# Optimization experiments

Measured on AMD Instinct MI355X. Metric: run time of the kernel, lower is better.

Reference implementation:

```python
import jax, jax.numpy as jnp
import numpy as np

V, E, HD, C, B, T = 30000, 256, 512, 9, 128, 256
H = HD // 2  # per-direction hidden size


def setup_inputs() -> dict:
    key = jax.random.key(0)
    ks = iter(jax.random.split(key, 64))

    def rn(shape, scale):
        return jax.random.normal(next(ks), shape, jnp.float32) * scale

    s = 1.0 / np.sqrt(H)
    inp = {}
    inp["x"] = jax.random.randint(next(ks), (B, T), 0, V, dtype=jnp.int32)
    inp["tags"] = jax.random.randint(next(ks), (B, T), 0, C, dtype=jnp.int32)
    inp["mask"] = jnp.ones((B, T), dtype=bool)
    inp["emb"] = rn((V, E), 1.0)
    in_dims = [E, HD]
    for l in range(2):
        for d in ("f", "b"):
            inp[f"w_ih_l{l}{d}"] = rn((4 * H, in_dims[l]), s)
            inp[f"w_hh_l{l}{d}"] = rn((4 * H, H), s)
            inp[f"b_ih_l{l}{d}"] = rn((4 * H,), s)
            inp[f"b_hh_l{l}{d}"] = rn((4 * H,), s)
    inp["lin_w"] = rn((C, HD), 1.0 / np.sqrt(HD))
    inp["lin_b"] = rn((C,), 0.01)
    inp["trans"] = rn((C, C), 0.1)
    inp["start"] = rn((C,), 0.1)
    inp["end"] = rn((C,), 0.1)
    return inp


def _lstm_dir(x, w_ih, w_hh, b_ih, b_hh):
    # x: [T, B, in]; PyTorch gate order i, f, g, o
    Bn = x.shape[1]
    Hn = w_hh.shape[1]

    def step(carry, xt):
        h, c = carry
        g = xt @ w_ih.T + b_ih + h @ w_hh.T + b_hh
        i, f, gg, o = jnp.split(g, 4, axis=-1)
        c = jax.nn.sigmoid(f) * c + jax.nn.sigmoid(i) * jnp.tanh(gg)
        h = jax.nn.sigmoid(o) * jnp.tanh(c)
        return (h, c), h

    z = jnp.zeros((Bn, Hn), x.dtype)
    _, hs = jax.lax.scan(step, (z, z), x)
    return hs  # [T, B, H]


def _bilstm(x, pf, pb):
    hf = _lstm_dir(x, *pf)
    hb = _lstm_dir(x[::-1], *pb)[::-1]
    return jnp.concatenate([hf, hb], axis=-1)  # [T, B, 2H]


def _crf_nll(em, tags, mask, trans, start, end):
    # em: [T, B, C] (time-major emissions); tags, mask: [B, T]
    tags_t = tags.T              # [T, B]
    mf = mask.astype(em.dtype).T  # [T, B]
    Bn = tags.shape[0]
    bidx = jnp.arange(Bn)
    # numerator: score of the gold path
    num = start[tags_t[0]] + em[0, bidx, tags_t[0]]
    step_em = jnp.take_along_axis(em[1:], tags_t[1:, :, None], axis=2)[..., 0]  # [T-1, B]
    step_sc = trans[tags_t[:-1], tags_t[1:]] + step_em
    num = num + (step_sc * mf[1:]).sum(0)
    lengths = mask.sum(1).astype(jnp.int32)
    last_tags = tags[bidx, lengths - 1]
    num = num + end[last_tags]
    # denominator: forward algorithm (logsumexp scan over time)
    alpha0 = start + em[0]  # [B, C]

    def step(alpha, inp):
        e, m = inp
        nxt = jax.nn.logsumexp(alpha[:, :, None] + trans[None] + e[:, None, :], axis=1)
        return jnp.where(m[:, None] > 0, nxt, alpha), None

    alpha, _ = jax.lax.scan(step, alpha0, (em[1:], mf[1:]))
    logZ = jax.nn.logsumexp(alpha + end, axis=1)
    return -(num - logZ).mean()


def reference(x, tags, mask, emb,
              w_ih_l0f, w_hh_l0f, b_ih_l0f, b_hh_l0f,
              w_ih_l0b, w_hh_l0b, b_ih_l0b, b_hh_l0b,
              w_ih_l1f, w_hh_l1f, b_ih_l1f, b_hh_l1f,
              w_ih_l1b, w_hh_l1b, b_ih_l1b, b_hh_l1b,
              lin_w, lin_b, trans, start, end):
    xt = emb[x].transpose(1, 0, 2)  # [T, B, E]
    h1 = _bilstm(xt, (w_ih_l0f, w_hh_l0f, b_ih_l0f, b_hh_l0f),
                 (w_ih_l0b, w_hh_l0b, b_ih_l0b, b_hh_l0b))
    h2 = _bilstm(h1, (w_ih_l1f, w_hh_l1f, b_ih_l1f, b_hh_l1f),
                 (w_ih_l1b, w_hh_l1b, b_ih_l1b, b_hh_l1b))
    em = h2 @ lin_w.T + lin_b  # [T, B, C]
    return _crf_nll(em, tags, mask, trans, start, end)
```

## Files before the change

kernel.cpp:

```cpp
#include <hip/hip_runtime.h>

#define T_LEN 256
#define B_SZ  128
#define E_DIM 256
#define NC    9

typedef short bf16x8 __attribute__((ext_vector_type(8)));
typedef float f32x4  __attribute__((ext_vector_type(4)));
typedef unsigned short u16x4 __attribute__((ext_vector_type(4)));
typedef unsigned int   u32x2 __attribute__((ext_vector_type(2)));

__device__ __forceinline__ float bf2f(unsigned short u) {
    return __uint_as_float(((unsigned)u) << 16);
}
__device__ __forceinline__ unsigned short f2bf(float f) {
    unsigned x = __float_as_uint(f);
    unsigned r = x + 0x7FFFu + ((x >> 16) & 1u);
    return (unsigned short)(r >> 16);
}
__device__ __forceinline__ float rcpf(float x) { return __builtin_amdgcn_rcpf(x); }
__device__ __forceinline__ float sigf(float x) { return rcpf(1.0f + __expf(-x)); }
__device__ __forceinline__ float tanh_fast(float x) {
    float e = __expf(2.0f * x);
    return 1.0f - 2.0f * rcpf(e + 1.0f);
}

__global__ void k_prep(const float* __restrict__ i0f, const float* __restrict__ i0b,
                       const float* __restrict__ i1f, const float* __restrict__ i1b,
                       const float* __restrict__ h0, const float* __restrict__ h1,
                       const float* __restrict__ h2, const float* __restrict__ h3,
                       unsigned short* __restrict__ d0f, unsigned short* __restrict__ d0b,
                       unsigned short* __restrict__ d1f, unsigned short* __restrict__ d1b,
                       unsigned short* __restrict__ p0, unsigned short* __restrict__ p1,
                       unsigned short* __restrict__ p2, unsigned short* __restrict__ p3) {
    int j = blockIdx.y;
    int idx = blockIdx.x * 256 + threadIdx.x;
    if (j < 4) {
        int n = (j < 2) ? 262144 : 524288;
        if (idx < n) {
            const float* s = (j == 0) ? i0f : (j == 1) ? i0b : (j == 2) ? i1f : i1b;
            unsigned short* d = (j == 0) ? d0f : (j == 1) ? d0b : (j == 2) ? d1f : d1b;
            d[idx] = f2bf(s[idx]);
        }
    } else {
        if (idx < 262144) {
            const float* s = (j == 4) ? h0 : (j == 5) ? h1 : (j == 6) ? h2 : h3;
            unsigned short* d = (j == 4) ? p0 : (j == 5) ? p1 : (j == 6) ? p2 : p3;
            int p = idx >> 8, k = idx & 255;
            int srow = ((p >> 4) & 3) * 256 + (p >> 9) * 128 + ((p >> 6) & 7) * 16 + (p & 15);
            d[idx] = f2bf(s[srow * 256 + k]);
        }
    }
}

__global__ void k_bias4(const float* __restrict__ a0, const float* __restrict__ b0,
                        const float* __restrict__ a1, const float* __restrict__ b1,
                        const float* __restrict__ a2, const float* __restrict__ b2,
                        const float* __restrict__ a3, const float* __restrict__ b3,
                        float* __restrict__ d) {
    int idx = blockIdx.x * 256 + threadIdx.x;
    if (idx < 4096) {
        int j = idx >> 10, i = idx & 1023;
        const float* a = (j == 0) ? a0 : (j == 1) ? a1 : (j == 2) ? a2 : a3;
        const float* b = (j == 0) ? b0 : (j == 1) ? b1 : (j == 2) ? b2 : b3;
        d[idx] = a[i] + b[i];
    }
}

__global__ void k_init(unsigned* __restrict__ c) {
    int i = blockIdx.x * 256 + threadIdx.x;
    if (i < 2048)
        __hip_atomic_store(c + i, 0u, __ATOMIC_RELAXED, __HIP_MEMORY_SCOPE_AGENT);
}

__global__ void k_embed(const int* __restrict__ x, const float* __restrict__ emb,
                        unsigned short* __restrict__ X0) {
    int row = blockIdx.x * 4 + (threadIdx.x >> 6);
    int lane = threadIdx.x & 63;
    int t = row >> 7, b = row & 127;
    int xi = x[b * T_LEN + t];
    const float4 e = *reinterpret_cast<const float4*>(emb + (size_t)xi * E_DIM + lane * 4);
    ushort4 o;
    o.x = f2bf(e.x); o.y = f2bf(e.y); o.z = f2bf(e.z); o.w = f2bf(e.w);
    *reinterpret_cast<ushort4*>(X0 + (size_t)row * E_DIM + lane * 4) = o;
}

template<int K>
__global__ __launch_bounds__(256, 1) void k_gemm2(const unsigned short* __restrict__ A,
                                                  const unsigned short* __restrict__ W,
                                                  const float* __restrict__ bias,
                                                  unsigned short* __restrict__ out) {
    int m0 = blockIdx.x * 128;
    int w = threadIdx.x >> 6, l = threadIdx.x & 63;
    int lr = l & 15, hi = l >> 4;
    bf16x8 af[2][K / 32];
#pragma unroll
    for (int s = 0; s < 2; s++)
#pragma unroll
        for (int kk = 0; kk < K / 32; kk++)
            af[s][kk] = *reinterpret_cast<const bf16x8*>(
                A + (size_t)(m0 + w * 32 + s * 16 + lr) * K + kk * 32 + hi * 8);
#pragma unroll 1
    for (int tn = 0; tn < 16; tn++) {
        int n0 = tn * 64;
        f32x4 acc[4][2];
        f32x4 z = {0.f, 0.f, 0.f, 0.f};
#pragma unroll
        for (int c = 0; c < 4; c++) { acc[c][0] = z; acc[c][1] = z; }
#pragma unroll
        for (int kk = 0; kk < K / 32; kk++) {
#pragma unroll
            for (int c = 0; c < 4; c++) {
                bf16x8 wf = *reinterpret_cast<const bf16x8*>(
                    W + (size_t)(n0 + c * 16 + lr) * K + kk * 32 + hi * 8);
                acc[c][0] = __builtin_amdgcn_mfma_f32_16x16x32_bf16(wf, af[0][kk], acc[c][0], 0, 0, 0);
                acc[c][1] = __builtin_amdgcn_mfma_f32_16x16x32_bf16(wf, af[1][kk], acc[c][1], 0, 0, 0);
            }
        }
#pragma unroll
        for (int c = 0; c < 4; c++) {
            float4 bv = *reinterpret_cast<const float4*>(bias + n0 + c * 16 + hi * 4);
#pragma unroll
            for (int s = 0; s < 2; s++) {
                unsigned short hb[4];
                hb[0] = f2bf(acc[c][s][0] + bv.x);
                hb[1] = f2bf(acc[c][s][1] + bv.y);
                hb[2] = f2bf(acc[c][s][2] + bv.z);
                hb[3] = f2bf(acc[c][s][3] + bv.w);
                u32x2 dv;
                dv[0] = (unsigned)hb[0] | ((unsigned)hb[1] << 16);
                dv[1] = (unsigned)hb[2] | ((unsigned)hb[3] << 16);
                *reinterpret_cast<u32x2*>(out + (size_t)(m0 + w * 32 + s * 16 + lr) * 1024
                                          + n0 + c * 16 + hi * 4) = dv;
            }
        }
    }
}

__global__ __launch_bounds__(512, 1) void k_lstm7(const unsigned short* __restrict__ Gf,
                                                  const unsigned short* __restrict__ Gb,
                                                  const unsigned short* __restrict__ Wpf,
                                                  const unsigned short* __restrict__ Wpb,
                                                  unsigned short* __restrict__ Hout,
                                                  unsigned* __restrict__ flags_base) {
    __shared__ unsigned short smem[12288];
    unsigned short* gin_lds = smem;
    unsigned short* h_lds = smem + 8192;

    int bx = blockIdx.x;
    int dir = (bx >> 3) & 1, rg = bx & 7, sidx = bx >> 4;
    const unsigned short* G = dir ? Gb : Gf;
    const unsigned short* Wp = dir ? Wpb : Wpf;

    unsigned long long myflag = (unsigned long long)(uintptr_t)(flags_base + bx * 16);
    unsigned long long pflag  = (unsigned long long)(uintptr_t)(flags_base + (bx ^ 16) * 16);

    int tid = threadIdx.x;
    int w = tid >> 6, l = tid & 63;
    int lr = l & 15, hi = l >> 4;
    int hc4 = sidx * 128 + w * 16 + hi * 4;

    bf16x8 wfr[4][8];
    {
        const unsigned short* wbase = Wp + (size_t)(sidx * 8 + w) * 64 * 256;
#pragma unroll
        for (int g = 0; g < 4; g++)
#pragma unroll
            for (int kk = 0; kk < 8; kk++)
                wfr[g][kk] = *reinterpret_cast<const bf16x8*>(
                    wbase + (size_t)(g * 16 + lr) * 256 + kk * 32 + hi * 8);
    }

    int Xr = (lr & 7) << 4;
    int goff[2];
#pragma unroll
    for (int p = 0; p < 2; p++) {
        int off = (p * 512 + tid) * 16;
        int row = off >> 10, inrow = off & 1023;
        int g = inrow >> 8, cb = inrow & 255;
        int Xs = (row & 7) << 4;
        goff[p] = (rg * 16 + row) * 1024 + ((g * 512 + sidx * 256 + (cb ^ Xs)) >> 1);
    }
    int phoff = 0;
    {
        int off = (tid & 255) * 16;
        int prow = off >> 8, pin = off & 255;
        int Xs = (prow & 7) << 4;
        phoff = (rg * 16 + prow) * 512 + dir * 256 + (sidx ^ 1) * 128 + ((pin ^ Xs) >> 1);
    }
    int lofs[8];
#pragma unroll
    for (int kk = 0; kk < 8; kk++) {
        int cb = kk * 64 + hi * 16;
        lofs[kk] = (cb >> 8) * 4096 + lr * 256 + ((cb & 255) ^ Xr);
    }
    int wofs = sidx * 4096 + lr * 256 + ((w * 32 + hi * 8) ^ Xr);
    int gofs[4];
#pragma unroll
    for (int g = 0; g < 4; g++) gofs[g] = lr * 1024 + g * 256 + ((w * 32 + hi * 8) ^ Xr);

    int t0 = dir ? (T_LEN - 1) : 0;
    long dg = dir ? -(long)(B_SZ * 1024) : (long)(B_SZ * 1024);
    long dh = dir ? -(long)(B_SZ * 512)  : (long)(B_SZ * 512);
    const unsigned short* Gt  = G + (size_t)t0 * (B_SZ * 1024);
    const unsigned short* Hpt = Hout + (size_t)t0 * (B_SZ * 512);
    unsigned short* hst = Hout + ((size_t)t0 * B_SZ + rg * 16 + lr) * 512 + dir * 256 + hc4;

    float c4[4] = {0.f, 0.f, 0.f, 0.f};
    f32x4 z = {0.f, 0.f, 0.f, 0.f};

    for (int s = 0; s < T_LEN; s++) {
        __builtin_amdgcn_global_load_lds(
            (const __attribute__((address_space(1))) unsigned int*)(Gt + goff[0]),
            (__attribute__((address_space(3))) unsigned int*)(gin_lds + w * 512), 16, 0, 0);
        __builtin_amdgcn_global_load_lds(
            (const __attribute__((address_space(1))) unsigned int*)(Gt + goff[1]),
            (__attribute__((address_space(3))) unsigned int*)(gin_lds + 4096 + w * 512), 16, 0, 0);

        if (s == 0) {
            *reinterpret_cast<int4*>((char*)h_lds + tid * 16) = make_int4(0, 0, 0, 0);
        } else {
            if (tid == 0) {
                unsigned v;
                for (;;) {
                    asm volatile("global_load_dword %0, %1, off sc1\n\ts_waitcnt vmcnt(0)"
                                 : "=v"(v) : "v"(pflag) : "memory");
                    if (v >= (unsigned)s) break;
                    __builtin_amdgcn_s_sleep(1);
                }
            }
            __syncthreads();
            if (tid < 256) {
                __builtin_amdgcn_global_load_lds(
                    (const __attribute__((address_space(1))) unsigned int*)(Hpt + phoff),
                    (__attribute__((address_space(3))) unsigned int*)(h_lds + (sidx ^ 1) * 2048 + w * 512),
                    16, 0, 0);
            }
            Hpt += dh;
        }
        asm volatile("s_waitcnt vmcnt(0)" ::: "memory");
        __syncthreads();

        bf16x8 hf[8];
#pragma unroll
        for (int kk = 0; kk < 8; kk++)
            hf[kk] = *reinterpret_cast<const bf16x8*>((char*)h_lds + lofs[kk]);
        f32x4 acc[4];
#pragma unroll
        for (int g = 0; g < 4; g++) acc[g] = z;
#pragma unroll
        for (int g = 0; g < 4; g++)
#pragma unroll
            for (int kk = 0; kk < 8; kk++)
                acc[g] = __builtin_amdgcn_mfma_f32_16x16x32_bf16(wfr[g][kk], hf[kk], acc[g], 0, 0, 0);
        __syncthreads();

        u16x4 g4[4];
#pragma unroll
        for (int g = 0; g < 4; g++)
            g4[g] = *reinterpret_cast<const u16x4*>((char*)gin_lds + gofs[g]);
        unsigned short hb[4];
#pragma unroll
        for (int r = 0; r < 4; r++) {
            float xi = acc[0][r] + bf2f(g4[0][r]);
            float xf = acc[1][r] + bf2f(g4[1][r]);
            float xg = acc[2][r] + bf2f(g4[2][r]);
            float xo = acc[3][r] + bf2f(g4[3][r]);
            float cv = sigf(xf) * c4[r] + sigf(xi) * tanh_fast(xg);
            c4[r] = cv;
            hb[r] = f2bf(sigf(xo) * tanh_fast(cv));
        }
        u32x2 dv;
        dv[0] = (unsigned)hb[0] | ((unsigned)hb[1] << 16);
        dv[1] = (unsigned)hb[2] | ((unsigned)hb[3] << 16);
        *reinterpret_cast<u32x2*>((char*)h_lds + wofs) = dv;
        unsigned long long saddr = (unsigned long long)(uintptr_t)hst;
        asm volatile("global_store_dwordx2 %0, %1, off sc1" :: "v"(saddr), "v"(dv));
        hst += dh;

        asm volatile("s_waitcnt vmcnt(0)" ::: "memory");
        __syncthreads();
        if (tid == 0) {
            unsigned val = (unsigned)(s + 1);
            asm volatile("global_store_dword %0, %1, off sc1" :: "v"(myflag), "v"(val));
        }
        Gt += dg;
    }
}

__global__ __launch_bounds__(256) void k_emis(const unsigned short* __restrict__ H2,
                                              const float* __restrict__ lw,
                                              const float* __restrict__ lb,
                                              float* __restrict__ EM) {
    int row = blockIdx.x * 4 + (threadIdx.x >> 6);
    int lane = threadIdx.x & 63;
    bf16x8 hv = *reinterpret_cast<const bf16x8*>(H2 + (size_t)row * 512 + lane * 8);
    float hf[8];
#pragma unroll
    for (int j = 0; j < 8; j++) hf[j] = bf2f((unsigned short)hv[j]);
#pragma unroll
    for (int cc = 0; cc < NC; cc++) {
        const float* wr = lw + cc * 512 + lane * 8;
        float4 w0 = *reinterpret_cast<const float4*>(wr);
        float4 w1 = *reinterpret_cast<const float4*>(wr + 4);
        float d = hf[0] * w0.x + hf[1] * w0.y + hf[2] * w0.z + hf[3] * w0.w +
                  hf[4] * w1.x + hf[5] * w1.y + hf[6] * w1.z + hf[7] * w1.w;
#pragma unroll
        for (int off = 32; off >= 1; off >>= 1) d += __shfl_down(d, off, 64);
        if (lane == 0) EM[(size_t)row * NC + cc] = d + lb[cc];
    }
}

__global__ __launch_bounds__(64) void k_crf(const float* __restrict__ EM,
                                            const int* __restrict__ tags,
                                            const float* __restrict__ trans,
                                            const float* __restrict__ start,
                                            const float* __restrict__ end,
                                            float* __restrict__ partials) {
    int b = blockIdx.x, tid = threadIdx.x;
    __shared__ float tr[160];
    for (int i = tid; i < 160; i += 64) tr[i] = (i < 81) ? trans[i] : 0.f;
    __syncthreads();

    int j = tid;
    float alpha = -1e30f;
    if (j < 9) alpha = start[j] + EM[b * NC + j];

    for (int t = 1; t < T_LEN; t++) {
        float av[9];
#pragma unroll
        for (int i = 0; i < 9; i++) av[i] = __shfl(alpha, i, 64) + tr[i * 9 + j];
        float m = av[0];
#pragma unroll
        for (int i = 1; i < 9; i++) m = fmaxf(m, av[i]);
        float sum = 0.f;
#pragma unroll
        for (int i = 0; i < 9; i++) sum += expf(av[i] - m);
        float e = (j < 9) ? EM[(size_t)t * (B_SZ * NC) + b * NC + j] : 0.f;
        float na = m + logf(sum) + e;
        alpha = (j < 9) ? na : -1e30f;
    }
    float aend[9];
    float m2 = -1e30f;
#pragma unroll
    for (int i = 0; i < 9; i++) {
        aend[i] = __shfl(alpha, i, 64) + end[i];
        m2 = fmaxf(m2, aend[i]);
    }
    float s2 = 0.f;
#pragma unroll
    for (int i = 0; i < 9; i++) s2 += expf(aend[i] - m2);
    float logZ = m2 + logf(s2);

    float nsum = 0.f;
    for (int t = 1 + tid; t < T_LEN; t += 64) {
        int tp = tags[b * T_LEN + t - 1], tc = tags[b * T_LEN + t];
        nsum += tr[tp * 9 + tc] + EM[(size_t)t * (B_SZ * NC) + b * NC + tc];
    }
#pragma unroll
    for (int off = 32; off >= 1; off >>= 1) nsum += __shfl_down(nsum, off, 64);

    if (tid == 0) {
        int t0 = tags[b * T_LEN], tl = tags[b * T_LEN + T_LEN - 1];
        float num = start[t0] + EM[b * NC + t0] + nsum + end[tl];
        partials[b] = num - logZ;
    }
}

__global__ void k_reduce(const float* __restrict__ partials, float* __restrict__ out) {
    int tid = threadIdx.x;
    float v = partials[tid];
#pragma unroll
    for (int off = 32; off >= 1; off >>= 1) v += __shfl_down(v, off, 64);
    __shared__ float sm[2];
    if ((tid & 63) == 0) sm[tid >> 6] = v;
    __syncthreads();
    if (tid == 0) out[0] = -(sm[0] + sm[1]) / 128.0f;
}

extern "C" void kernel_launch(void* const* d_in, const int* in_sizes, int n_in,
                              void* d_out, int out_size, void* d_ws, size_t ws_size,
                              hipStream_t stream) {
    const int*   x     = (const int*)d_in[0];
    const int*   tags  = (const int*)d_in[1];
    const float* emb   = (const float*)d_in[3];
    const float* w_ih[4] = {(const float*)d_in[4],  (const float*)d_in[8],
                            (const float*)d_in[12], (const float*)d_in[16]};
    const float* w_hh[4] = {(const float*)d_in[5],  (const float*)d_in[9],
                            (const float*)d_in[13], (const float*)d_in[17]};
    const float* b_ih[4] = {(const float*)d_in[6],  (const float*)d_in[10],
                            (const float*)d_in[14], (const float*)d_in[18]};
    const float* b_hh[4] = {(const float*)d_in[7],  (const float*)d_in[11],
                            (const float*)d_in[15], (const float*)d_in[19]};
    const float* lin_w = (const float*)d_in[20];
    const float* lin_b = (const float*)d_in[21];
    const float* trans = (const float*)d_in[22];
    const float* start = (const float*)d_in[23];
    const float* endv  = (const float*)d_in[24];

    char* ws = (char*)d_ws;
    size_t off = 0;
    auto alloc = [&](size_t bytes) -> void* {
        size_t a = (off + 255) & ~(size_t)255;
        off = a + bytes;
        return (void*)(ws + a);
    };

    unsigned short* wb_ih0f = (unsigned short*)alloc(1024 * 256 * 2);
    unsigned short* wb_ih0b = (unsigned short*)alloc(1024 * 256 * 2);
    unsigned short* wb_ih1f = (unsigned short*)alloc(1024 * 512 * 2);
    unsigned short* wb_ih1b = (unsigned short*)alloc(1024 * 512 * 2);
    unsigned short* wp0f = (unsigned short*)alloc(1024 * 256 * 2);
    unsigned short* wp0b = (unsigned short*)alloc(1024 * 256 * 2);
    unsigned short* wp1f = (unsigned short*)alloc(1024 * 256 * 2);
    unsigned short* wp1b = (unsigned short*)alloc(1024 * 256 * 2);
    float* bsum = (float*)alloc(4096 * 4);
    unsigned short* X0 = (unsigned short*)alloc((size_t)32768 * 256 * 2);
    unsigned short* Gf = (unsigned short*)alloc((size_t)32768 * 1024 * 2);
    unsigned short* Gb = (unsigned short*)alloc((size_t)32768 * 1024 * 2);
    unsigned short* H1 = (unsigned short*)alloc((size_t)32768 * 512 * 2);
    unsigned short* H2 = (unsigned short*)alloc((size_t)32768 * 512 * 2);
    float* EM = (float*)alloc((size_t)32768 * NC * 4);
    float* partials = (float*)alloc(128 * 4);
    unsigned* ctrs = (unsigned*)alloc(8192);

    hipLaunchKernelGGL(k_init, dim3(8), dim3(256), 0, stream, ctrs);

    hipLaunchKernelGGL(k_prep, dim3(2048, 8), dim3(256), 0, stream,
                       w_ih[0], w_ih[1], w_ih[2], w_ih[3],
                       w_hh[0], w_hh[1], w_hh[2], w_hh[3],
                       wb_ih0f, wb_ih0b, wb_ih1f, wb_ih1b,
                       wp0f, wp0b, wp1f, wp1b);
    hipLaunchKernelGGL(k_bias4, dim3(16), dim3(256), 0, stream,
                       b_ih[0], b_hh[0], b_ih[1], b_hh[1],
                       b_ih[2], b_hh[2], b_ih[3], b_hh[3], bsum);

    hipLaunchKernelGGL(k_embed, dim3(8192), dim3(256), 0, stream, x, emb, X0);

    hipLaunchKernelGGL(k_gemm2<256>, dim3(256), dim3(256), 0, stream, X0, wb_ih0f, bsum, Gf);
    hipLaunchKernelGGL(k_gemm2<256>, dim3(256), dim3(256), 0, stream, X0, wb_ih0b, bsum + 1024, Gb);
    hipLaunchKernelGGL(k_lstm7, dim3(32), dim3(512), 0, stream, Gf, Gb, wp0f, wp0b, H1, ctrs);

    hipLaunchKernelGGL(k_gemm2<512>, dim3(256), dim3(256), 0, stream, H1, wb_ih1f, bsum + 2048, Gf);
    hipLaunchKernelGGL(k_gemm2<512>, dim3(256), dim3(256), 0, stream, H1, wb_ih1b, bsum + 3072, Gb);
    hipLaunchKernelGGL(k_lstm7, dim3(32), dim3(512), 0, stream, Gf, Gb, wp1f, wp1b, H2, ctrs + 1024);

    hipLaunchKernelGGL(k_emis, dim3(8192), dim3(256), 0, stream, H2, lin_w, lin_b, EM);
    hipLaunchKernelGGL(k_crf, dim3(128), dim3(64), 0, stream, EM, tags, trans, start, endv, partials);
    hipLaunchKernelGGL(k_reduce, dim3(1), dim3(128), 0, stream, partials, (float*)d_out);
}
```

Before: 2.053 ms.

## Run each LSTM direction/row-group in one 1024-thread block, removing cross-block flags

The recurrent LSTM kernel previously split the hidden dimension across two 512-thread blocks that exchanged h through global memory with spin-wait flags every timestep. Now one 1024-thread block covers the full hidden size per (direction, row group), keeping h entirely in double-buffered LDS, and prefetches the next timestep's gate inputs into a second LDS buffer. This removes the per-step global flag polling, the h exchange, and the flag-init kernel, and it changes the recurrent weight permutation to match the new layout. In exchange only 16 blocks run, with higher register pressure per block and 80KB of LDS each.

```diff
diff --git a/kernel.cpp b/kernel.cpp
--- a/kernel.cpp
+++ b/kernel.cpp
@@ -47,7 +47,7 @@
             const float* s = (j == 4) ? h0 : (j == 5) ? h1 : (j == 6) ? h2 : h3;
             unsigned short* d = (j == 4) ? p0 : (j == 5) ? p1 : (j == 6) ? p2 : p3;
             int p = idx >> 8, k = idx & 255;
-            int srow = ((p >> 4) & 3) * 256 + (p >> 9) * 128 + ((p >> 6) & 7) * 16 + (p & 15);
+            int srow = ((p >> 4) & 3) * 256 + (p >> 6) * 16 + (p & 15);
             d[idx] = f2bf(s[srow * 256 + k]);
         }
     }
@@ -65,12 +65,6 @@
         const float* b = (j == 0) ? b0 : (j == 1) ? b1 : (j == 2) ? b2 : b3;
         d[idx] = a[i] + b[i];
     }
-}
-
-__global__ void k_init(unsigned* __restrict__ c) {
-    int i = blockIdx.x * 256 + threadIdx.x;
-    if (i < 2048)
-        __hip_atomic_store(c + i, 0u, __ATOMIC_RELAXED, __HIP_MEMORY_SCOPE_AGENT);
 }
 
 __global__ void k_embed(const int* __restrict__ x, const float* __restrict__ emb,
@@ -137,32 +131,27 @@
     }
 }
 
-__global__ __launch_bounds__(512, 1) void k_lstm7(const unsigned short* __restrict__ Gf,
-                                                  const unsigned short* __restrict__ Gb,
-                                                  const unsigned short* __restrict__ Wpf,
-                                                  const unsigned short* __restrict__ Wpb,
-                                                  unsigned short* __restrict__ Hout,
-                                                  unsigned* __restrict__ flags_base) {
-    __shared__ unsigned short smem[12288];
-    unsigned short* gin_lds = smem;
-    unsigned short* h_lds = smem + 8192;
+__global__ __launch_bounds__(1024, 1) void k_lstm8(const unsigned short* __restrict__ Gf,
+                                                   const unsigned short* __restrict__ Gb,
+                                                   const unsigned short* __restrict__ Wpf,
+                                                   const unsigned short* __restrict__ Wpb,
+                                                   unsigned short* __restrict__ Hout) {
+    __shared__ unsigned short smem[40960];
+    unsigned short* gbuf = smem;
+    unsigned short* hbuf = smem + 32768;
 
     int bx = blockIdx.x;
-    int dir = (bx >> 3) & 1, rg = bx & 7, sidx = bx >> 4;
+    int dir = bx >> 3, rg = bx & 7;
     const unsigned short* G = dir ? Gb : Gf;
     const unsigned short* Wp = dir ? Wpb : Wpf;
-
-    unsigned long long myflag = (unsigned long long)(uintptr_t)(flags_base + bx * 16);
-    unsigned long long pflag  = (unsigned long long)(uintptr_t)(flags_base + (bx ^ 16) * 16);
 
     int tid = threadIdx.x;
     int w = tid >> 6, l = tid & 63;
     int lr = l & 15, hi = l >> 4;
-    int hc4 = sidx * 128 + w * 16 + hi * 4;
 
     bf16x8 wfr[4][8];
     {
-        const unsigned short* wbase = Wp + (size_t)(sidx * 8 + w) * 64 * 256;
+        const unsigned short* wbase = Wp + (size_t)w * 64 * 256;
 #pragma unroll
         for (int g = 0; g < 4; g++)
 #pragma unroll
@@ -171,80 +160,60 @@
                     wbase + (size_t)(g * 16 + lr) * 256 + kk * 32 + hi * 8);
     }
 
-    int Xr = (lr & 7) << 4;
-    int goff[2];
-#pragma unroll
-    for (int p = 0; p < 2; p++) {
-        int off = (p * 512 + tid) * 16;
-        int row = off >> 10, inrow = off & 1023;
-        int g = inrow >> 8, cb = inrow & 255;
-        int Xs = (row & 7) << 4;
-        goff[p] = (rg * 16 + row) * 1024 + ((g * 512 + sidx * 256 + (cb ^ Xs)) >> 1);
-    }
-    int phoff = 0;
-    {
-        int off = (tid & 255) * 16;
-        int prow = off >> 8, pin = off & 255;
-        int Xs = (prow & 7) << 4;
-        phoff = (rg * 16 + prow) * 512 + dir * 256 + (sidx ^ 1) * 128 + ((pin ^ Xs) >> 1);
-    }
-    int lofs[8];
-#pragma unroll
-    for (int kk = 0; kk < 8; kk++) {
-        int cb = kk * 64 + hi * 16;
-        lofs[kk] = (cb >> 8) * 4096 + lr * 256 + ((cb & 255) ^ Xr);
-    }
-    int wofs = sidx * 4096 + lr * 256 + ((w * 32 + hi * 8) ^ Xr);
-    int gofs[4];
-#pragma unroll
-    for (int g = 0; g < 4; g++) gofs[g] = lr * 1024 + g * 256 + ((w * 32 + hi * 8) ^ Xr);
+    int off0 = tid * 16, off1 = 16384 + tid * 16;
+    int r0 = off0 >> 11, in0 = off0 & 2047;
+    int r1 = off1 >> 11, in1 = off1 & 2047;
+    int gsrc0 = (rg * 16 + r0) * 1024 + ((in0 ^ ((r0 & 7) << 4)) >> 1);
+    int gsrc1 = (rg * 16 + r1) * 1024 + ((in1 ^ ((r1 & 7) << 4)) >> 1);
+    int Xs = (lr & 7) << 4, Xh = (lr & 15) << 4;
+    int hfo[8];
+#pragma unroll
+    for (int kk = 0; kk < 8; kk++) hfo[kk] = lr * 512 + ((kk * 64 + hi * 16) ^ Xh);
+    int gro[4];
+#pragma unroll
+    for (int g = 0; g < 4; g++) gro[g] = lr * 2048 + ((g * 512 + w * 32 + hi * 8) ^ Xs);
+    int hwo = lr * 512 + ((w * 32 + hi * 8) ^ Xh);
 
     int t0 = dir ? (T_LEN - 1) : 0;
     long dg = dir ? -(long)(B_SZ * 1024) : (long)(B_SZ * 1024);
     long dh = dir ? -(long)(B_SZ * 512)  : (long)(B_SZ * 512);
-    const unsigned short* Gt  = G + (size_t)t0 * (B_SZ * 1024);
-    const unsigned short* Hpt = Hout + (size_t)t0 * (B_SZ * 512);
-    unsigned short* hst = Hout + ((size_t)t0 * B_SZ + rg * 16 + lr) * 512 + dir * 256 + hc4;
+    const unsigned short* G0 = G + (size_t)t0 * (B_SZ * 1024);
+    const unsigned short* Gpre = G0 + dg;
+    unsigned short* hst = Hout + ((size_t)t0 * B_SZ + rg * 16 + lr) * 512
+                          + dir * 256 + w * 16 + hi * 4;
+
+    *reinterpret_cast<int4*>((char*)hbuf + tid * 16) = make_int4(0, 0, 0, 0);
+    __builtin_amdgcn_global_load_lds(
+        (const __attribute__((address_space(1))) unsigned int*)(G0 + gsrc0),
+        (__attribute__((address_space(3))) unsigned int*)(gbuf + w * 512), 16, 0, 0);
+    __builtin_amdgcn_global_load_lds(
+        (const __attribute__((address_space(1))) unsigned int*)(G0 + gsrc1),
+        (__attribute__((address_space(3))) unsigned int*)(gbuf + 8192 + w * 512), 16, 0, 0);
+    __syncthreads();
 
     float c4[4] = {0.f, 0.f, 0.f, 0.f};
     f32x4 z = {0.f, 0.f, 0.f, 0.f};
 
-    for (int s = 0; s < T_LEN; s++) {
-        __builtin_amdgcn_global_load_lds(
-            (const __attribute__((address_space(1))) unsigned int*)(Gt + goff[0]),
-            (__attribute__((address_space(3))) unsigned int*)(gin_lds + w * 512), 16, 0, 0);
-        __builtin_amdgcn_global_load_lds(
-            (const __attribute__((address_space(1))) unsigned int*)(Gt + goff[1]),
-            (__attribute__((address_space(3))) unsigned int*)(gin_lds + 4096 + w * 512), 16, 0, 0);
-
-        if (s == 0) {
-            *reinterpret_cast<int4*>((char*)h_lds + tid * 16) = make_int4(0, 0, 0, 0);
-        } else {
-            if (tid == 0) {
-                unsigned v;
-                for (;;) {
-                    asm volatile("global_load_dword %0, %1, off sc1\n\ts_waitcnt vmcnt(0)"
-                                 : "=v"(v) : "v"(pflag) : "memory");
-                    if (v >= (unsigned)s) break;
-                    __builtin_amdgcn_s_sleep(1);
-                }
-            }
-            __syncthreads();
-            if (tid < 256) {
-                __builtin_amdgcn_global_load_lds(
-                    (const __attribute__((address_space(1))) unsigned int*)(Hpt + phoff),
-                    (__attribute__((address_space(3))) unsigned int*)(h_lds + (sidx ^ 1) * 2048 + w * 512),
-                    16, 0, 0);
-            }
-            Hpt += dh;
-        }
-        asm volatile("s_waitcnt vmcnt(0)" ::: "memory");
-        __syncthreads();
+    for (int s = 0; s < T_LEN; ++s) {
+        int rdg = (s & 1) * 16384;
+        int rdh = (s & 1) * 8192;
+
+        if (s < T_LEN - 1) {
+            unsigned short* dst = gbuf + (16384 - rdg);
+            __builtin_amdgcn_global_load_lds(
+                (const __attribute__((address_space(1))) unsigned int*)(Gpre + gsrc0),
+                (__attribute__((address_space(3))) unsigned int*)(dst + w * 512), 16, 0, 0);
+            __builtin_amdgcn_global_load_lds(
+                (const __attribute__((address_space(1))) unsigned int*)(Gpre + gsrc1),
+                (__attribute__((address_space(3))) unsigned int*)(dst + 8192 + w * 512), 16, 0, 0);
+            Gpre += dg;
+        }
 
         bf16x8 hf[8];
+        char* hrb = (char*)hbuf + rdh;
 #pragma unroll
         for (int kk = 0; kk < 8; kk++)
-            hf[kk] = *reinterpret_cast<const bf16x8*>((char*)h_lds + lofs[kk]);
+            hf[kk] = *reinterpret_cast<const bf16x8*>(hrb + hfo[kk]);
         f32x4 acc[4];
 #pragma unroll
         for (int g = 0; g < 4; g++) acc[g] = z;
@@ -253,12 +222,12 @@
 #pragma unroll
             for (int kk = 0; kk < 8; kk++)
                 acc[g] = __builtin_amdgcn_mfma_f32_16x16x32_bf16(wfr[g][kk], hf[kk], acc[g], 0, 0, 0);
-        __syncthreads();
-
+
+        char* grb = (char*)(gbuf + rdg);
         u16x4 g4[4];
 #pragma unroll
         for (int g = 0; g < 4; g++)
-            g4[g] = *reinterpret_cast<const u16x4*>((char*)gin_lds + gofs[g]);
+            g4[g] = *reinterpret_cast<const u16x4*>(grb + gro[g]);
         unsigned short hb[4];
 #pragma unroll
         for (int r = 0; r < 4; r++) {
@@ -273,18 +242,12 @@
         u32x2 dv;
         dv[0] = (unsigned)hb[0] | ((unsigned)hb[1] << 16);
         dv[1] = (unsigned)hb[2] | ((unsigned)hb[3] << 16);
-        *reinterpret_cast<u32x2*>((char*)h_lds + wofs) = dv;
-        unsigned long long saddr = (unsigned long long)(uintptr_t)hst;
-        asm volatile("global_store_dwordx2 %0, %1, off sc1" :: "v"(saddr), "v"(dv));
+
+        *reinterpret_cast<u32x2*>((char*)hbuf + (8192 - rdh) + hwo) = dv;
+        *reinterpret_cast<u32x2*>(hst) = dv;
         hst += dh;
 
-        asm volatile("s_waitcnt vmcnt(0)" ::: "memory");
         __syncthreads();
-        if (tid == 0) {
-            unsigned val = (unsigned)(s + 1);
-            asm volatile("global_store_dword %0, %1, off sc1" :: "v"(myflag), "v"(val));
-        }
-        Gt += dg;
     }
 }
 
@@ -422,9 +385,6 @@
     unsigned short* H2 = (unsigned short*)alloc((size_t)32768 * 512 * 2);
     float* EM = (float*)alloc((size_t)32768 * NC * 4);
     float* partials = (float*)alloc(128 * 4);
-    unsigned* ctrs = (unsigned*)alloc(8192);
-
-    hipLaunchKernelGGL(k_init, dim3(8), dim3(256), 0, stream, ctrs);
 
     hipLaunchKernelGGL(k_prep, dim3(2048, 8), dim3(256), 0, stream,
                        w_ih[0], w_ih[1], w_ih[2], w_ih[3],
@@ -439,11 +399,11 @@
 
     hipLaunchKernelGGL(k_gemm2<256>, dim3(256), dim3(256), 0, stream, X0, wb_ih0f, bsum, Gf);
     hipLaunchKernelGGL(k_gemm2<256>, dim3(256), dim3(256), 0, stream, X0, wb_ih0b, bsum + 1024, Gb);
-    hipLaunchKernelGGL(k_lstm7, dim3(32), dim3(512), 0, stream, Gf, Gb, wp0f, wp0b, H1, ctrs);
+    hipLaunchKernelGGL(k_lstm8, dim3(16), dim3(1024), 0, stream, Gf, Gb, wp0f, wp0b, H1);
 
     hipLaunchKernelGGL(k_gemm2<512>, dim3(256), dim3(256), 0, stream, H1, wb_ih1f, bsum + 2048, Gf);
     hipLaunchKernelGGL(k_gemm2<512>, dim3(256), dim3(256), 0, stream, H1, wb_ih1b, bsum + 3072, Gb);
-    hipLaunchKernelGGL(k_lstm7, dim3(32), dim3(512), 0, stream, Gf, Gb, wp1f, wp1b, H2, ctrs + 1024);
+    hipLaunchKernelGGL(k_lstm8, dim3(16), dim3(1024), 0, stream, Gf, Gb, wp1f, wp1b, H2);
 
     hipLaunchKernelGGL(k_emis, dim3(8192), dim3(256), 0, stream, H2, lin_w, lin_b, EM);
     hipLaunchKernelGGL(k_crf, dim3(128), dim3(64), 0, stream, EM, tags, trans, start, endv, partials);
```

Measured after the change: 4.073 ms. +98.4%, slower.
